# Optimization experiments

Hardware: AMD Instinct MI355X
Metric: run time of the kernel (lower is better)

Reference implementation:

```python
import jax, jax.numpy as jnp
import numpy as np
import math

B, Q, K, D = 16, 2048, 2048, 128


def setup_inputs() -> dict:
    key = jax.random.key(0)
    kq, kk, kv, kl = jax.random.split(key, 4)
    queries = jax.random.normal(kq, (B, Q, D), dtype=jnp.float32)
    keys = jax.random.normal(kk, (B, K, D), dtype=jnp.float32)
    values = jax.random.normal(kv, (B, K, D), dtype=jnp.float32)
    valid_lens = jax.random.randint(kl, (B,), 1, K + 1, dtype=jnp.int32)
    return {"queries": queries, "keys": keys, "values": values, "valid_lens": valid_lens}


def reference(queries, keys, values, valid_lens):
    d = queries.shape[-1]
    # scores = bmm(Q, K^T) // sqrt(d)  -- source uses floor-division, kept faithfully
    scores = jnp.floor(jnp.einsum('bqd,bkd->bqk', queries, keys) / math.sqrt(d))
    # masked_softmax: positions >= valid_len[b] get -1e6 before softmax
    mask = jnp.arange(keys.shape[1]) < valid_lens[:, None, None]  # [B,1,K]
    scores = jnp.where(mask, scores, -1e6)
    attn = jax.nn.softmax(scores, axis=-1)
    # dropout in eval mode = identity
    return jnp.einsum('bqk,bkv->bqv', attn, values)
```

## Files before the change

### kernel.cpp

```cpp
#include <hip/hip_runtime.h>
#include <cmath>

typedef __attribute__((ext_vector_type(4))) float f32x4;
typedef __attribute__((ext_vector_type(8))) _Float16 f16x8;
typedef __attribute__((ext_vector_type(4))) _Float16 f16x4;

#define B_SZ 16
#define Q_SZ 2048
#define K_SZ 2048
#define D_SZ 128
#define BQ   128
#define BKT  64
#define PST  72
#define SCL  0.08838834764831845f
#define BUFSZ 49152

#define GLDS16(g, s) __builtin_amdgcn_global_load_lds(                      \
    (const __attribute__((address_space(1))) unsigned int*)(g),             \
    (__attribute__((address_space(3))) unsigned int*)(s), 16, 0, 0)

__global__ __launch_bounds__(256) void prep_all(
    const float* __restrict__ K, const float* __restrict__ V,
    _Float16* __restrict__ Khi, _Float16* __restrict__ Klo,
    _Float16* __restrict__ Vt)
{
  __shared__ _Float16 tmp[64][136];
  const int tid = threadIdx.x;
  if (blockIdx.x < 2048) {
    const int gid = blockIdx.x * 256 + tid;
    const int r = gid >> 4;
    const int g = gid & 15;
    const float* src = K + (size_t)r * D_SZ + g * 8;
    f16x8 hi, lo;
#pragma unroll
    for (int i = 0; i < 8; ++i) {
      float x = src[i];
      _Float16 h = (_Float16)x;
      hi[i] = h;
      lo[i] = (_Float16)((x - (float)h) * 2048.0f);
    }
    const size_t o = (size_t)r * D_SZ + ((g ^ (r & 7)) * 8);
    *(f16x8*)(Khi + o) = hi;
    *(f16x8*)(Klo + o) = lo;
  } else {
    const int vb = blockIdx.x - 2048;
    const int b = vb >> 5;
    const int k0 = (vb & 31) * 64;
    const float* Vb = V + ((size_t)b * K_SZ + k0) * D_SZ;
#pragma unroll
    for (int j = 0; j < 8; ++j) {
      const int e = j * 1024 + tid * 4;
      const int k = e >> 7, d = e & 127;
      const f32x4 v = *(const f32x4*)(Vb + (size_t)k * D_SZ + d);
      f16x4 h;
#pragma unroll
      for (int i = 0; i < 4; ++i) h[i] = (_Float16)v[i];
      *(f16x4*)&tmp[k][d] = h;
    }
    __syncthreads();
#pragma unroll
    for (int i = 0; i < 4; ++i) {
      const int id = i * 256 + tid;
      const int gk = id >> 7, d = id & 127;
      f16x8 o;
#pragma unroll
      for (int jj = 0; jj < 8; ++jj) o[jj] = tmp[gk * 8 + jj][d];
      _Float16* dst = Vt + ((size_t)b * D_SZ + d) * K_SZ + k0 + ((gk ^ (d & 7)) * 8);
      *(f16x8*)dst = o;
    }
  }
}

__global__ __launch_bounds__(512, 2) void attn(
    const float* __restrict__ Qm, const _Float16* __restrict__ KhiG,
    const _Float16* __restrict__ KloG, const _Float16* __restrict__ VtG,
    const int* __restrict__ vlp, float* __restrict__ Om,
    float* __restrict__ P1, float* __restrict__ L0, float* __restrict__ L1,
    unsigned* __restrict__ cnt, const int split)
{
  __shared__ __align__(16) char sm[2 * BUFSZ + BQ * PST * 2];
  _Float16* smP = (_Float16*)(sm + 2 * BUFSZ);
  __shared__ int s_task;
  __shared__ float Ls[4][2][32];

  const int tid  = threadIdx.x;
  const int wave = tid >> 6;
  const int lane = tid & 63;
  const int ln   = lane & 15;
  const int quad = lane >> 4;
  const int qh   = wave >> 1;
  const int kh   = wave & 1;

  for (;;) {
    int t;
    if (split) {
      if (tid == 0) s_task = (int)atomicAdd(cnt, 1u);
      __syncthreads();
      t = s_task;
      __syncthreads();
      if (t >= 512) return;
    } else {
      t = blockIdx.x;
    }

    int half = 0, b, qt;
    if (split) { half = (t >= 256); const int u = t & 255; b = u >> 4; qt = u & 15; }
    else       { b = t >> 4; qt = t & 15; }
    const int q0     = qt * BQ;
    const int valid  = vlp[b];
    const int kstart = half * 1024;
    const int kend   = split ? min(valid, kstart + 1024) : valid;
    if (kend <= kstart) { if (!split) return; continue; }
    const int ntiles = (kend - kstart + BKT - 1) / BKT;

    const float* Qb    = Qm + (size_t)b * Q_SZ * D_SZ;
    const char*  gKhiB = (const char*)KhiG + (size_t)b * K_SZ * 256;
    const char*  gKloB = (const char*)KloG + (size_t)b * K_SZ * 256;
    const char*  gVtB  = (const char*)VtG  + (size_t)b * D_SZ * (K_SZ * 2);

    auto STAGE = [&](int k0g, char* buf) {
      const char* gh = gKhiB + (size_t)k0g * 256;
      const char* gl = gKloB + (size_t)k0g * 256;
#pragma unroll
      for (int i = 0; i < 2; ++i) {
        const int off = wave * 1024 + i * 8192;
        GLDS16(gh + off + lane * 16, buf + off);
      }
#pragma unroll
      for (int i = 0; i < 2; ++i) {
        const int off = wave * 1024 + i * 8192;
        GLDS16(gl + off + lane * 16, buf + 16384 + off);
      }
#pragma unroll
      for (int i = 0; i < 2; ++i) {
        const int off = wave * 1024 + i * 8192;
        const int a = off + lane * 16;
        const int d = a >> 7, win = a & 127;
        GLDS16(gVtB + (size_t)d * (K_SZ * 2) + (size_t)k0g * 2 + win,
               buf + 32768 + off);
      }
    };

    f16x8 qhi[2][4], qlo[2][4];
#pragma unroll
    for (int mt = 0; mt < 2; ++mt) {
      const int qrow = q0 + qh * 32 + mt * 16 + ln;
      const float* srcb = Qb + (size_t)qrow * D_SZ + quad * 8;
#pragma unroll
      for (int c = 0; c < 4; ++c) {
#pragma unroll
        for (int j = 0; j < 8; ++j) {
          float x = srcb[c * 32 + j];
          _Float16 h = (_Float16)x;
          qhi[mt][c][j] = h;
          qlo[mt][c][j] = (_Float16)((x - (float)h) * 2048.0f);
        }
      }
    }

    const f32x4 vzero = {0.f, 0.f, 0.f, 0.f};
    f32x4 accO[2][4];
    float lsum[8];
#pragma unroll
    for (int mt = 0; mt < 2; ++mt)
#pragma unroll
      for (int nb = 0; nb < 4; ++nb) accO[mt][nb] = vzero;
#pragma unroll
    for (int i = 0; i < 8; ++i) lsum[i] = 0.0f;

    STAGE(kstart, sm);

    for (int kt = 0; kt < ntiles; ++kt) {
      char* cbuf = sm + (kt & 1) * BUFSZ;
      _Float16* smKhi = (_Float16*)cbuf;
      _Float16* smKlo = (_Float16*)(cbuf + 16384);
      _Float16* smVt  = (_Float16*)(cbuf + 32768);
      const int k0g = kstart + kt * BKT;

      if (kt + 1 < ntiles) {
        STAGE(kstart + (kt + 1) * BKT, sm + ((kt + 1) & 1) * BUFSZ);
        asm volatile("s_waitcnt vmcnt(6)" ::: "memory");
      } else {
        asm volatile("s_waitcnt vmcnt(0)" ::: "memory");
      }
      __builtin_amdgcn_sched_barrier(0);
      __builtin_amdgcn_s_barrier();
      __builtin_amdgcn_sched_barrier(0);

      f32x4 accM[2][2], accC[2][2];
#pragma unroll
      for (int mt = 0; mt < 2; ++mt)
#pragma unroll
        for (int nb = 0; nb < 2; ++nb) { accM[mt][nb] = vzero; accC[mt][nb] = vzero; }
      __builtin_amdgcn_s_setprio(1);
#pragma unroll
      for (int nb = 0; nb < 2; ++nb) {
        const int row = kh * 32 + nb * 16 + ln;
        const _Float16* bh_base = smKhi + row * 128;
        const _Float16* bl_base = smKlo + row * 128;
#pragma unroll
        for (int c = 0; c < 4; ++c) {
          const int pg = (((c * 4 + quad) ^ (ln & 7)) * 8);
          const f16x8 bh = *(const f16x8*)(bh_base + pg);
          const f16x8 bl = *(const f16x8*)(bl_base + pg);
#pragma unroll
          for (int mt = 0; mt < 2; ++mt) {
            accM[mt][nb] = __builtin_amdgcn_mfma_f32_16x16x32_f16(qhi[mt][c], bh, accM[mt][nb], 0, 0, 0);
            accC[mt][nb] = __builtin_amdgcn_mfma_f32_16x16x32_f16(qhi[mt][c], bl, accC[mt][nb], 0, 0, 0);
            accC[mt][nb] = __builtin_amdgcn_mfma_f32_16x16x32_f16(qlo[mt][c], bh, accC[mt][nb], 0, 0, 0);
          }
        }
      }
      __builtin_amdgcn_s_setprio(0);

#pragma unroll
      for (int nb = 0; nb < 2; ++nb) {
        const int  key = k0g + kh * 32 + nb * 16 + ln;
        const bool ok  = key < valid;
#pragma unroll
        for (int mt = 0; mt < 2; ++mt) {
#pragma unroll
          for (int r = 0; r < 4; ++r) {
            const float s = accM[mt][nb][r] + accC[mt][nb][r] * (1.0f / 2048.0f);
            const float e = ok ? __expf(floorf(s * SCL)) : 0.0f;
            lsum[mt * 4 + r] += e;
            smP[(qh * 32 + mt * 16 + quad * 4 + r) * PST + kh * 32 + nb * 16 + ln] = (_Float16)e;
          }
        }
      }
      asm volatile("s_waitcnt lgkmcnt(0)" ::: "memory");
      __builtin_amdgcn_sched_barrier(0);
      __builtin_amdgcn_s_barrier();
      __builtin_amdgcn_sched_barrier(0);

      __builtin_amdgcn_s_setprio(1);
#pragma unroll
      for (int c = 0; c < 2; ++c) {
        f16x8 af[2];
#pragma unroll
        for (int mt = 0; mt < 2; ++mt)
          af[mt] = *(const f16x8*)(smP + (qh * 32 + mt * 16 + ln) * PST + c * 32 + quad * 8);
#pragma unroll
        for (int nb = 0; nb < 4; ++nb) {
          const int drow = kh * 64 + nb * 16 + ln;
          const int pg = (((c * 4 + quad) ^ (ln & 7)) * 8);
          const f16x8 bf = *(const f16x8*)(smVt + drow * 64 + pg);
#pragma unroll
          for (int mt = 0; mt < 2; ++mt)
            accO[mt][nb] = __builtin_amdgcn_mfma_f32_16x16x32_f16(af[mt], bf, accO[mt][nb], 0, 0, 0);
        }
      }
      __builtin_amdgcn_s_setprio(0);
      asm volatile("s_waitcnt lgkmcnt(0)" ::: "memory");
      __builtin_amdgcn_sched_barrier(0);
      __builtin_amdgcn_s_barrier();
      __builtin_amdgcn_sched_barrier(0);
    }

#pragma unroll
    for (int i = 0; i < 8; ++i) {
      float v = lsum[i];
      v += __shfl_xor(v, 1, 64);
      v += __shfl_xor(v, 2, 64);
      v += __shfl_xor(v, 4, 64);
      v += __shfl_xor(v, 8, 64);
      lsum[i] = v;
    }

    if (split) {
      float* Lh = half ? L1 : L0;
      if (ln == 0) {
#pragma unroll
        for (int mt = 0; mt < 2; ++mt)
#pragma unroll
          for (int r = 0; r < 4; ++r)
            atomicAdd(Lh + b * Q_SZ + q0 + qh * 32 + mt * 16 + quad * 4 + r, lsum[mt * 4 + r]);
      }
      float* dst = (half ? P1 : Om) + ((size_t)(b * Q_SZ + q0)) * D_SZ;
#pragma unroll
      for (int mt = 0; mt < 2; ++mt)
#pragma unroll
        for (int nb = 0; nb < 4; ++nb)
#pragma unroll
          for (int r = 0; r < 4; ++r)
            dst[(size_t)(qh * 32 + mt * 16 + quad * 4 + r) * D_SZ + kh * 64 + nb * 16 + ln] =
                accO[mt][nb][r];
    } else {
      if (ln == 0) {
#pragma unroll
        for (int mt = 0; mt < 2; ++mt)
#pragma unroll
          for (int r = 0; r < 4; ++r)
            Ls[qh][kh][mt * 16 + quad * 4 + r] = lsum[mt * 4 + r];
      }
      __syncthreads();
      float* Ob = Om + (size_t)b * Q_SZ * D_SZ;
#pragma unroll
      for (int mt = 0; mt < 2; ++mt) {
#pragma unroll
        for (int r = 0; r < 4; ++r) {
          const int rr = mt * 16 + quad * 4 + r;
          const float inv = 1.0f / (Ls[qh][0][rr] + Ls[qh][1][rr]);
#pragma unroll
          for (int nb = 0; nb < 4; ++nb)
            Ob[(size_t)(q0 + qh * 32 + rr) * D_SZ + kh * 64 + nb * 16 + ln] =
                accO[mt][nb][r] * inv;
        }
      }
    }
    if (!split) return;
  }
}

__global__ __launch_bounds__(256) void finalize(
    float* __restrict__ Om, const float* __restrict__ P1,
    const float* __restrict__ L0, const float* __restrict__ L1,
    const int* __restrict__ vlp)
{
  const int idx = blockIdx.x * 256 + threadIdx.x;
  const size_t e = (size_t)idx * 4;
  const int row = (int)(e >> 7);
  const int b = row >> 11;
  const int valid = vlp[b];
  f32x4 o = *(const f32x4*)(Om + e);
  float l = L0[row];
  if (valid > 1024) {
    const f32x4 p = *(const f32x4*)(P1 + e);
    o += p;
    l += L1[row];
  }
  const float inv = 1.0f / l;
  o *= inv;
  *(f32x4*)(Om + e) = o;
}

extern "C" void kernel_launch(void* const* d_in, const int* in_sizes, int n_in,
                              void* d_out, int out_size, void* d_ws, size_t ws_size,
                              hipStream_t stream) {
  const float* Qm = (const float*)d_in[0];
  const float* Km = (const float*)d_in[1];
  const float* Vm = (const float*)d_in[2];
  const int*   vl = (const int*)d_in[3];
  float*       Om = (float*)d_out;

  const size_t elems = (size_t)B_SZ * K_SZ * D_SZ;
  const size_t PREP  = 3 * elems * sizeof(_Float16);
  const size_t HDR   = 262400;
  const size_t P1SZ  = elems * sizeof(float);
  char* W = (char*)d_ws;

  if (ws_size >= HDR + PREP + P1SZ) {
    unsigned* cnt = (unsigned*)W;
    float*    L0  = (float*)(W + 256);
    float*    L1  = (float*)(W + 256 + 131072);
    _Float16* Khi = (_Float16*)(W + HDR);
    _Float16* Klo = Khi + elems;
    _Float16* Vt  = Klo + elems;
    float*    P1  = (float*)(W + HDR + PREP);
    hipMemsetAsync(d_ws, 0, HDR, stream);
    prep_all<<<2560, 256, 0, stream>>>(Km, Vm, Khi, Klo, Vt);
    attn<<<256, 512, 0, stream>>>(Qm, Khi, Klo, Vt, vl, Om, P1, L0, L1, cnt, 1);
    finalize<<<4096, 256, 0, stream>>>(Om, P1, L0, L1, vl);
  } else {
    _Float16* Khi = (_Float16*)W;
    _Float16* Klo = Khi + elems;
    _Float16* Vt  = Klo + elems;
    prep_all<<<2560, 256, 0, stream>>>(Km, Vm, Khi, Klo, Vt);
    attn<<<256, 512, 0, stream>>>(Qm, Khi, Klo, Vt, vl, Om,
                                  nullptr, nullptr, nullptr, nullptr, 0);
  }
}
```

Measured before the change: 172.3 us.

## Keep softmax probabilities in registers via transposed QK MFMA, drop P shared-memory round trip

The attention kernel is restructured from 8 waves (split across query and key halves) to 4 waves, each owning 32 query rows and all 128 output dims. QK^T is computed with operands swapped so the resulting score layout can be packed directly into the A-operand of the PV MFMA, which removes the shared-memory P buffer and its barrier. The V transpose in prep is permuted to match the new key ordering. Staging is re-pipelined with separate Khi (double-buffered), Klo and V buffers in 64 KB of LDS. Each wave now holds more accumulators, which raises register pressure and reduces the number of waves available to hide latency.

```diff
diff --git a/kernel.cpp b/kernel.cpp
--- a/kernel.cpp
+++ b/kernel.cpp
@@ -4,6 +4,7 @@
 typedef __attribute__((ext_vector_type(4))) float f32x4;
 typedef __attribute__((ext_vector_type(8))) _Float16 f16x8;
 typedef __attribute__((ext_vector_type(4))) _Float16 f16x4;
+typedef __attribute__((ext_vector_type(4))) unsigned int u32x4;
 
 #define B_SZ 16
 #define Q_SZ 2048
@@ -11,13 +12,17 @@
 #define D_SZ 128
 #define BQ   128
 #define BKT  64
-#define PST  72
 #define SCL  0.08838834764831845f
-#define BUFSZ 49152
 
 #define GLDS16(g, s) __builtin_amdgcn_global_load_lds(                      \
     (const __attribute__((address_space(1))) unsigned int*)(g),             \
     (__attribute__((address_space(3))) unsigned int*)(s), 16, 0, 0)
+
+static __device__ inline unsigned pk16(float a, float b) {
+  unsigned short ha = __builtin_bit_cast(unsigned short, (_Float16)a);
+  unsigned short hb = __builtin_bit_cast(unsigned short, (_Float16)b);
+  return (unsigned)ha | ((unsigned)hb << 16);
+}
 
 __global__ __launch_bounds__(256) void prep_all(
     const float* __restrict__ K, const float* __restrict__ V,
@@ -64,32 +69,32 @@
       const int gk = id >> 7, d = id & 127;
       f16x8 o;
 #pragma unroll
-      for (int jj = 0; jj < 8; ++jj) o[jj] = tmp[gk * 8 + jj][d];
+      for (int jj = 0; jj < 8; ++jj) {
+        const int kap = ((gk >> 2) << 5) | ((jj >> 2) << 4) | ((gk & 3) << 2) | (jj & 3);
+        o[jj] = tmp[kap][d];
+      }
       _Float16* dst = Vt + ((size_t)b * D_SZ + d) * K_SZ + k0 + ((gk ^ (d & 7)) * 8);
       *(f16x8*)dst = o;
     }
   }
 }
 
-__global__ __launch_bounds__(512, 2) void attn(
+__global__ __launch_bounds__(256, 2) void attn(
     const float* __restrict__ Qm, const _Float16* __restrict__ KhiG,
     const _Float16* __restrict__ KloG, const _Float16* __restrict__ VtG,
     const int* __restrict__ vlp, float* __restrict__ Om,
     float* __restrict__ P1, float* __restrict__ L0, float* __restrict__ L1,
     unsigned* __restrict__ cnt, const int split)
 {
-  __shared__ __align__(16) char sm[2 * BUFSZ + BQ * PST * 2];
-  _Float16* smP = (_Float16*)(sm + 2 * BUFSZ);
+  __shared__ __align__(16) char sm[65536];
+  __shared__ float Ls[128];
   __shared__ int s_task;
-  __shared__ float Ls[4][2][32];
 
   const int tid  = threadIdx.x;
   const int wave = tid >> 6;
   const int lane = tid & 63;
   const int ln   = lane & 15;
   const int quad = lane >> 4;
-  const int qh   = wave >> 1;
-  const int kh   = wave & 1;
 
   for (;;) {
     int t;
@@ -118,33 +123,39 @@
     const char*  gKloB = (const char*)KloG + (size_t)b * K_SZ * 256;
     const char*  gVtB  = (const char*)VtG  + (size_t)b * D_SZ * (K_SZ * 2);
 
-    auto STAGE = [&](int k0g, char* buf) {
-      const char* gh = gKhiB + (size_t)k0g * 256;
-      const char* gl = gKloB + (size_t)k0g * 256;
-#pragma unroll
-      for (int i = 0; i < 2; ++i) {
-        const int off = wave * 1024 + i * 8192;
-        GLDS16(gh + off + lane * 16, buf + off);
-      }
-#pragma unroll
-      for (int i = 0; i < 2; ++i) {
-        const int off = wave * 1024 + i * 8192;
-        GLDS16(gl + off + lane * 16, buf + 16384 + off);
-      }
-#pragma unroll
-      for (int i = 0; i < 2; ++i) {
-        const int off = wave * 1024 + i * 8192;
+    auto SThi = [&](int k0g, int sel) {
+      const char* g = gKhiB + (size_t)k0g * 256;
+      char* d = sm + sel * 16384;
+#pragma unroll
+      for (int i = 0; i < 4; ++i) {
+        const int off = wave * 1024 + i * 4096;
+        GLDS16(g + off + lane * 16, d + off);
+      }
+    };
+    auto STlo = [&](int k0g) {
+      const char* g = gKloB + (size_t)k0g * 256;
+      char* d = sm + 32768;
+#pragma unroll
+      for (int i = 0; i < 4; ++i) {
+        const int off = wave * 1024 + i * 4096;
+        GLDS16(g + off + lane * 16, d + off);
+      }
+    };
+    auto STv = [&](int k0g) {
+      char* dst = sm + 49152;
+#pragma unroll
+      for (int i = 0; i < 4; ++i) {
+        const int off = wave * 1024 + i * 4096;
         const int a = off + lane * 16;
         const int d = a >> 7, win = a & 127;
-        GLDS16(gVtB + (size_t)d * (K_SZ * 2) + (size_t)k0g * 2 + win,
-               buf + 32768 + off);
+        GLDS16(gVtB + (size_t)d * (K_SZ * 2) + (size_t)k0g * 2 + win, dst + off);
       }
     };
 
     f16x8 qhi[2][4], qlo[2][4];
 #pragma unroll
     for (int mt = 0; mt < 2; ++mt) {
-      const int qrow = q0 + qh * 32 + mt * 16 + ln;
+      const int qrow = q0 + wave * 32 + mt * 16 + ln;
       const float* srcb = Qb + (size_t)qrow * D_SZ + quad * 8;
 #pragma unroll
       for (int c = 0; c < 4; ++c) {
@@ -159,139 +170,141 @@
     }
 
     const f32x4 vzero = {0.f, 0.f, 0.f, 0.f};
-    f32x4 accO[2][4];
-    float lsum[8];
+    f32x4 accO[2][8];
+    float lsum[2] = {0.f, 0.f};
 #pragma unroll
     for (int mt = 0; mt < 2; ++mt)
 #pragma unroll
-      for (int nb = 0; nb < 4; ++nb) accO[mt][nb] = vzero;
-#pragma unroll
-    for (int i = 0; i < 8; ++i) lsum[i] = 0.0f;
-
-    STAGE(kstart, sm);
+      for (int dt = 0; dt < 8; ++dt) accO[mt][dt] = vzero;
+
+    SThi(kstart, 0);
+    STlo(kstart);
 
     for (int kt = 0; kt < ntiles; ++kt) {
-      char* cbuf = sm + (kt & 1) * BUFSZ;
-      _Float16* smKhi = (_Float16*)cbuf;
-      _Float16* smKlo = (_Float16*)(cbuf + 16384);
-      _Float16* smVt  = (_Float16*)(cbuf + 32768);
       const int k0g = kstart + kt * BKT;
-
-      if (kt + 1 < ntiles) {
-        STAGE(kstart + (kt + 1) * BKT, sm + ((kt + 1) & 1) * BUFSZ);
-        asm volatile("s_waitcnt vmcnt(6)" ::: "memory");
+      _Float16* smKhi = (_Float16*)(sm + (kt & 1) * 16384);
+      _Float16* smKlo = (_Float16*)(sm + 32768);
+      _Float16* smVt  = (_Float16*)(sm + 49152);
+      const bool more = (kt + 1 < ntiles);
+
+      STv(k0g);
+      if (more) {
+        SThi(k0g + BKT, (kt + 1) & 1);
+        asm volatile("s_waitcnt vmcnt(8)" ::: "memory");
+      } else {
+        asm volatile("s_waitcnt vmcnt(4)" ::: "memory");
+      }
+      __builtin_amdgcn_sched_barrier(0);
+      __builtin_amdgcn_s_barrier();
+      __builtin_amdgcn_sched_barrier(0);
+
+      f16x8 pa[2][2];
+#pragma unroll
+      for (int hk = 0; hk < 2; ++hk) {
+        f32x4 accM[2][2], accC[2][2];
+#pragma unroll
+        for (int mt = 0; mt < 2; ++mt)
+#pragma unroll
+          for (int nb2 = 0; nb2 < 2; ++nb2) { accM[mt][nb2] = vzero; accC[mt][nb2] = vzero; }
+        __builtin_amdgcn_s_setprio(1);
+#pragma unroll
+        for (int nb2 = 0; nb2 < 2; ++nb2) {
+          const int row = (hk * 2 + nb2) * 16 + ln;
+          const _Float16* bh_base = smKhi + row * 128;
+          const _Float16* bl_base = smKlo + row * 128;
+#pragma unroll
+          for (int c = 0; c < 4; ++c) {
+            const int pg = (((c * 4 + quad) ^ (ln & 7)) * 8);
+            const f16x8 bh = *(const f16x8*)(bh_base + pg);
+            const f16x8 bl = *(const f16x8*)(bl_base + pg);
+#pragma unroll
+            for (int mt = 0; mt < 2; ++mt) {
+              accM[mt][nb2] = __builtin_amdgcn_mfma_f32_16x16x32_f16(bh, qhi[mt][c], accM[mt][nb2], 0, 0, 0);
+              accC[mt][nb2] = __builtin_amdgcn_mfma_f32_16x16x32_f16(bl, qhi[mt][c], accC[mt][nb2], 0, 0, 0);
+              accC[mt][nb2] = __builtin_amdgcn_mfma_f32_16x16x32_f16(bh, qlo[mt][c], accC[mt][nb2], 0, 0, 0);
+            }
+          }
+        }
+        __builtin_amdgcn_s_setprio(0);
+
+#pragma unroll
+        for (int mt = 0; mt < 2; ++mt) {
+          u32x4 w;
+#pragma unroll
+          for (int nb2 = 0; nb2 < 2; ++nb2) {
+            float e[4];
+#pragma unroll
+            for (int r = 0; r < 4; ++r) {
+              const int key = k0g + (hk * 2 + nb2) * 16 + quad * 4 + r;
+              const float s = accM[mt][nb2][r] + accC[mt][nb2][r] * (1.0f / 2048.0f);
+              e[r] = (key < valid) ? __expf(floorf(s * SCL)) : 0.0f;
+              lsum[mt] += e[r];
+            }
+            w[nb2 * 2 + 0] = pk16(e[0], e[1]);
+            w[nb2 * 2 + 1] = pk16(e[2], e[3]);
+          }
+          pa[mt][hk] = __builtin_bit_cast(f16x8, w);
+        }
+      }
+
+      if (more) {
+        asm volatile("s_waitcnt vmcnt(4)" ::: "memory");
       } else {
         asm volatile("s_waitcnt vmcnt(0)" ::: "memory");
       }
       __builtin_amdgcn_sched_barrier(0);
       __builtin_amdgcn_s_barrier();
       __builtin_amdgcn_sched_barrier(0);
-
-      f32x4 accM[2][2], accC[2][2];
-#pragma unroll
-      for (int mt = 0; mt < 2; ++mt)
-#pragma unroll
-        for (int nb = 0; nb < 2; ++nb) { accM[mt][nb] = vzero; accC[mt][nb] = vzero; }
+      if (more) STlo(k0g + BKT);
+
       __builtin_amdgcn_s_setprio(1);
 #pragma unroll
-      for (int nb = 0; nb < 2; ++nb) {
-        const int row = kh * 32 + nb * 16 + ln;
-        const _Float16* bh_base = smKhi + row * 128;
-        const _Float16* bl_base = smKlo + row * 128;
-#pragma unroll
-        for (int c = 0; c < 4; ++c) {
-          const int pg = (((c * 4 + quad) ^ (ln & 7)) * 8);
-          const f16x8 bh = *(const f16x8*)(bh_base + pg);
-          const f16x8 bl = *(const f16x8*)(bl_base + pg);
-#pragma unroll
-          for (int mt = 0; mt < 2; ++mt) {
-            accM[mt][nb] = __builtin_amdgcn_mfma_f32_16x16x32_f16(qhi[mt][c], bh, accM[mt][nb], 0, 0, 0);
-            accC[mt][nb] = __builtin_amdgcn_mfma_f32_16x16x32_f16(qhi[mt][c], bl, accC[mt][nb], 0, 0, 0);
-            accC[mt][nb] = __builtin_amdgcn_mfma_f32_16x16x32_f16(qlo[mt][c], bh, accC[mt][nb], 0, 0, 0);
-          }
-        }
-      }
-      __builtin_amdgcn_s_setprio(0);
-
-#pragma unroll
-      for (int nb = 0; nb < 2; ++nb) {
-        const int  key = k0g + kh * 32 + nb * 16 + ln;
-        const bool ok  = key < valid;
-#pragma unroll
-        for (int mt = 0; mt < 2; ++mt) {
-#pragma unroll
-          for (int r = 0; r < 4; ++r) {
-            const float s = accM[mt][nb][r] + accC[mt][nb][r] * (1.0f / 2048.0f);
-            const float e = ok ? __expf(floorf(s * SCL)) : 0.0f;
-            lsum[mt * 4 + r] += e;
-            smP[(qh * 32 + mt * 16 + quad * 4 + r) * PST + kh * 32 + nb * 16 + ln] = (_Float16)e;
-          }
-        }
-      }
-      asm volatile("s_waitcnt lgkmcnt(0)" ::: "memory");
-      __builtin_amdgcn_sched_barrier(0);
-      __builtin_amdgcn_s_barrier();
-      __builtin_amdgcn_sched_barrier(0);
-
-      __builtin_amdgcn_s_setprio(1);
-#pragma unroll
       for (int c = 0; c < 2; ++c) {
-        f16x8 af[2];
-#pragma unroll
-        for (int mt = 0; mt < 2; ++mt)
-          af[mt] = *(const f16x8*)(smP + (qh * 32 + mt * 16 + ln) * PST + c * 32 + quad * 8);
-#pragma unroll
-        for (int nb = 0; nb < 4; ++nb) {
-          const int drow = kh * 64 + nb * 16 + ln;
+#pragma unroll
+        for (int dt = 0; dt < 8; ++dt) {
+          const int drow = dt * 16 + ln;
           const int pg = (((c * 4 + quad) ^ (ln & 7)) * 8);
           const f16x8 bf = *(const f16x8*)(smVt + drow * 64 + pg);
 #pragma unroll
           for (int mt = 0; mt < 2; ++mt)
-            accO[mt][nb] = __builtin_amdgcn_mfma_f32_16x16x32_f16(af[mt], bf, accO[mt][nb], 0, 0, 0);
+            accO[mt][dt] = __builtin_amdgcn_mfma_f32_16x16x32_f16(pa[mt][c], bf, accO[mt][dt], 0, 0, 0);
         }
       }
       __builtin_amdgcn_s_setprio(0);
-      asm volatile("s_waitcnt lgkmcnt(0)" ::: "memory");
       __builtin_amdgcn_sched_barrier(0);
       __builtin_amdgcn_s_barrier();
       __builtin_amdgcn_sched_barrier(0);
     }
 
 #pragma unroll
-    for (int i = 0; i < 8; ++i) {
-      float v = lsum[i];
-      v += __shfl_xor(v, 1, 64);
-      v += __shfl_xor(v, 2, 64);
-      v += __shfl_xor(v, 4, 64);
-      v += __shfl_xor(v, 8, 64);
-      lsum[i] = v;
+    for (int mt = 0; mt < 2; ++mt) {
+      float v = lsum[mt];
+      v += __shfl_xor(v, 16, 64);
+      v += __shfl_xor(v, 32, 64);
+      lsum[mt] = v;
     }
 
     if (split) {
       float* Lh = half ? L1 : L0;
-      if (ln == 0) {
+      if (lane < 16) {
 #pragma unroll
         for (int mt = 0; mt < 2; ++mt)
+          atomicAdd(Lh + b * Q_SZ + q0 + wave * 32 + mt * 16 + lane, lsum[mt]);
+      }
+      float* dst = (half ? P1 : Om) + ((size_t)(b * Q_SZ + q0)) * D_SZ;
+#pragma unroll
+      for (int mt = 0; mt < 2; ++mt)
+#pragma unroll
+        for (int dt = 0; dt < 8; ++dt)
 #pragma unroll
           for (int r = 0; r < 4; ++r)
-            atomicAdd(Lh + b * Q_SZ + q0 + qh * 32 + mt * 16 + quad * 4 + r, lsum[mt * 4 + r]);
-      }
-      float* dst = (half ? P1 : Om) + ((size_t)(b * Q_SZ + q0)) * D_SZ;
-#pragma unroll
-      for (int mt = 0; mt < 2; ++mt)
-#pragma unroll
-        for (int nb = 0; nb < 4; ++nb)
-#pragma unroll
-          for (int r = 0; r < 4; ++r)
-            dst[(size_t)(qh * 32 + mt * 16 + quad * 4 + r) * D_SZ + kh * 64 + nb * 16 + ln] =
-                accO[mt][nb][r];
+            dst[(size_t)(wave * 32 + mt * 16 + quad * 4 + r) * D_SZ + dt * 16 + ln] =
+                accO[mt][dt][r];
     } else {
-      if (ln == 0) {
+      if (lane < 16) {
 #pragma unroll
         for (int mt = 0; mt < 2; ++mt)
-#pragma unroll
-          for (int r = 0; r < 4; ++r)
-            Ls[qh][kh][mt * 16 + quad * 4 + r] = lsum[mt * 4 + r];
+          Ls[wave * 32 + mt * 16 + lane] = lsum[mt];
       }
       __syncthreads();
       float* Ob = Om + (size_t)b * Q_SZ * D_SZ;
@@ -299,14 +312,14 @@
       for (int mt = 0; mt < 2; ++mt) {
 #pragma unroll
         for (int r = 0; r < 4; ++r) {
-          const int rr = mt * 16 + quad * 4 + r;
-          const float inv = 1.0f / (Ls[qh][0][rr] + Ls[qh][1][rr]);
-#pragma unroll
-          for (int nb = 0; nb < 4; ++nb)
-            Ob[(size_t)(q0 + qh * 32 + rr) * D_SZ + kh * 64 + nb * 16 + ln] =
-                accO[mt][nb][r] * inv;
-        }
-      }
+          const float inv = 1.0f / Ls[wave * 32 + mt * 16 + quad * 4 + r];
+#pragma unroll
+          for (int dt = 0; dt < 8; ++dt)
+            Ob[(size_t)(q0 + wave * 32 + mt * 16 + quad * 4 + r) * D_SZ + dt * 16 + ln] =
+                accO[mt][dt][r] * inv;
+        }
+      }
+      __syncthreads();
     }
     if (!split) return;
   }
@@ -359,14 +372,14 @@
     float*    P1  = (float*)(W + HDR + PREP);
     hipMemsetAsync(d_ws, 0, HDR, stream);
     prep_all<<<2560, 256, 0, stream>>>(Km, Vm, Khi, Klo, Vt);
-    attn<<<256, 512, 0, stream>>>(Qm, Khi, Klo, Vt, vl, Om, P1, L0, L1, cnt, 1);
+    attn<<<512, 256, 0, stream>>>(Qm, Khi, Klo, Vt, vl, Om, P1, L0, L1, cnt, 1);
     finalize<<<4096, 256, 0, stream>>>(Om, P1, L0, L1, vl);
   } else {
     _Float16* Khi = (_Float16*)W;
     _Float16* Klo = Khi + elems;
     _Float16* Vt  = Klo + elems;
     prep_all<<<2560, 256, 0, stream>>>(Km, Vm, Khi, Klo, Vt);
-    attn<<<256, 512, 0, stream>>>(Qm, Khi, Klo, Vt, vl, Om,
+    attn<<<256, 256, 0, stream>>>(Qm, Khi, Klo, Vt, vl, Om,
                                   nullptr, nullptr, nullptr, nullptr, 0);
   }
 }
```

Result: no change. 175.0 us (+1.6%).
